# Optimization experiments

Hardware: AMD Instinct MI355X
Metric: run time of the kernel (lower is better)

The kernel has to match this reference:

```python
import jax, jax.numpy as jnp
import numpy as np

B, L, D, H = 2, 1024, 1024, 16
DH = D // H
E, ES, K = 32, 128, 4
LN_EPS = 1e-5


def sinusoidal_pos(length, d):
    # relative offsets length-1 .. -(length-1), Transformer-XL convention
    pos = jnp.arange(length - 1, -length, -1, dtype=jnp.float32)  # [2L-1]
    inv = jnp.exp(-jnp.arange(0, d, 2, dtype=jnp.float32) * (np.log(10000.0) / d))
    ang = pos[:, None] * inv[None, :]
    return jnp.concatenate([jnp.sin(ang), jnp.cos(ang)], axis=-1)  # [2L-1, D]


def layer_norm(x, g, b):
    m = jnp.mean(x, -1, keepdims=True)
    v = jnp.mean(jnp.square(x - m), -1, keepdims=True)
    return (x - m) * jax.lax.rsqrt(v + LN_EPS) * g + b


def rel_attention(x, Wq, Wk, Wv, Wo, Wp):
    q = (x @ Wq).reshape(B, L, H, DH).transpose(0, 2, 1, 3)
    k = (x @ Wk).reshape(B, L, H, DH).transpose(0, 2, 1, 3)
    v = (x @ Wv).reshape(B, L, H, DH).transpose(0, 2, 1, 3)
    p = (sinusoidal_pos(L, D) @ Wp).reshape(2 * L - 1, H, DH).transpose(1, 0, 2)  # [H,2L-1,DH]
    ac = jnp.einsum('bhid,bhjd->bhij', q, k)            # content score
    bd = jnp.einsum('bhid,hpd->bhip', q, p)             # position score [B,H,L,2L-1]
    # offset index of key j relative to query i: pos array index = j - i + (L-1)
    idx = jnp.arange(L)[None, :] - jnp.arange(L)[:, None] + (L - 1)  # [L,L]
    bd = jnp.take_along_axis(bd, jnp.broadcast_to(idx[None, None], (B, H, L, L)), axis=-1)
    att = jax.nn.softmax((ac + bd) / np.sqrt(DH), axis=-1)
    out = jnp.einsum('bhij,bhjd->bhid', att, v).transpose(0, 2, 1, 3).reshape(B, L, D)
    return out @ Wo


def moe_ffn(x, sel_w, keys, values):
    t = x.reshape(-1, D)                                # [T, D]
    gates = jax.nn.sigmoid(t @ sel_w)                   # [T, E]
    topv, topi = jax.lax.top_k(gates, K)                # top-k expert selection
    gate = jnp.zeros_like(gates).at[jnp.arange(t.shape[0])[:, None], topi].set(topv)
    h = jax.nn.relu(jnp.einsum('td,edh->teh', t, keys))  # expert up-proj + ReLU
    y = jnp.einsum('teh,te,ehd->td', h, gate, values)    # gated expert down-proj
    return y.reshape(x.shape)


def setup_inputs():
    key = jax.random.key(0)
    ks = jax.random.split(key, 9)
    s = 0.02
    f32 = jnp.float32
    return {
        'src': jax.random.normal(ks[0], (B, L, D), f32),
        'Wq': jax.random.normal(ks[1], (D, D), f32) * s,
        'Wk': jax.random.normal(ks[2], (D, D), f32) * s,
        'Wv': jax.random.normal(ks[3], (D, D), f32) * s,
        'Wo': jax.random.normal(ks[4], (D, D), f32) * s,
        'Wp': jax.random.normal(ks[5], (D, D), f32) * s,
        'ln1_g': jnp.ones((D,), f32),
        'ln1_b': jnp.zeros((D,), f32),
        'ln2_g': jnp.ones((D,), f32),
        'ln2_b': jnp.zeros((D,), f32),
        'sel_w': jax.random.normal(ks[6], (D, E), f32) * s,
        'keys': jax.random.normal(ks[7], (E, D, ES), f32) * s,
        'values': jax.random.normal(ks[8], (E, ES, D), f32) * s,
    }


def reference(src, Wq, Wk, Wv, Wo, Wp, ln1_g, ln1_b, ln2_g, ln2_b, sel_w, keys, values):
    # pre-LN: attn block
    x2 = layer_norm(src, ln1_g, ln1_b)
    x = src + rel_attention(x2, Wq, Wk, Wv, Wo, Wp)
    # pre-LN: MoE FFN block
    x2 = layer_norm(x, ln2_g, ln2_b)
    return x + moe_ffn(x2, sel_w, keys, values)
```

## Files before the change

### kernel.cpp

```cpp
#include <hip/hip_runtime.h>
#include <hip/hip_bf16.h>
#include <cmath>

typedef __attribute__((ext_vector_type(8))) short s16x8;
typedef __attribute__((ext_vector_type(8))) __bf16 bf16x8;
typedef __attribute__((ext_vector_type(4))) float f32x4;

__device__ __forceinline__ float b2f(short u) {
  union { unsigned int u32; float f; } c;
  c.u32 = ((unsigned int)(unsigned short)u) << 16;
  return c.f;
}
__device__ __forceinline__ short f2b(float f) {
  __hip_bfloat16 h = __float2bfloat16(f);
  return *reinterpret_cast<short*>(&h);
}

__device__ __forceinline__ f32x4 mfma16(bf16x8 a, bf16x8 b, f32x4 c) {
  return __builtin_amdgcn_mfma_f32_16x16x32_bf16(a, b, c, 0, 0, 0);
}

__global__ __launch_bounds__(256) void conv_k(const float* __restrict__ in,
                                              short* __restrict__ out, int n) {
  int stride = gridDim.x << 8;
  for (int i = (blockIdx.x << 8) + threadIdx.x; i < n; i += stride)
    out[i] = f2b(in[i]);
}

__global__ __launch_bounds__(256) void pos_k(short* __restrict__ out) {
  int row = blockIdx.x;
  int t = threadIdx.x;
#pragma unroll
  for (int i = 0; i < 4; ++i) {
    int c = t + (i << 8);
    float val = 0.f;
    if (row < 2047) {
      int f = (c < 512) ? c : c - 512;
      float inv = expf(-(float)f * (float)(9.210340371976184 / 512.0));
      float ang = (float)(1023 - row) * inv;
      val = (c < 512) ? sinf(ang) : cosf(ang);
    }
    out[row * 1024 + c] = f2b(val);
  }
}

__global__ __launch_bounds__(256) void ln_k(const float* __restrict__ in,
                                            const float* __restrict__ g,
                                            const float* __restrict__ bb,
                                            short* __restrict__ out) {
  int row = blockIdx.x;
  int t = threadIdx.x;
  float v[4];
#pragma unroll
  for (int i = 0; i < 4; ++i) v[i] = in[row * 1024 + t + (i << 8)];
  __shared__ float red1[4], red2[4];
  float s = v[0] + v[1] + v[2] + v[3];
#pragma unroll
  for (int m = 1; m < 64; m <<= 1) s += __shfl_xor(s, m);
  if ((t & 63) == 0) red1[t >> 6] = s;
  __syncthreads();
  float mean = (red1[0] + red1[1] + red1[2] + red1[3]) * (1.f / 1024.f);
  float d2 = 0.f;
#pragma unroll
  for (int i = 0; i < 4; ++i) { float d = v[i] - mean; d2 += d * d; }
#pragma unroll
  for (int m = 1; m < 64; m <<= 1) d2 += __shfl_xor(d2, m);
  if ((t & 63) == 0) red2[t >> 6] = d2;
  __syncthreads();
  float var = (red2[0] + red2[1] + red2[2] + red2[3]) * (1.f / 1024.f);
  float rstd = rsqrtf(var + 1e-5f);
#pragma unroll
  for (int i = 0; i < 4; ++i) {
    int c = t + (i << 8);
    out[row * 1024 + c] = f2b((v[i] - mean) * rstd * g[c] + bb[c]);
  }
}

#define GD 1024
template <int EP>
__global__ __launch_bounds__(256) void gemm_k(const short* __restrict__ A,
                                              const short* __restrict__ B,
                                              void* __restrict__ outp,
                                              const float* __restrict__ resid) {
  __shared__ __align__(16) short lA[64 * 40];
  __shared__ __align__(16) short lB[64 * 40];
  const int tid = threadIdx.x;
  const int wave = tid >> 6, lane = tid & 63;
  const int wr = wave >> 1, wc = wave & 1;
  const int m0 = blockIdx.y * 64, n0 = blockIdx.x * 64;
  f32x4 acc[2][2] = {};
  const int ar = tid >> 2, ak = (tid & 3) << 3;
  const int bk = tid >> 3, bn = (tid & 7) << 3;
  const int k8 = (lane >> 4) << 3;
  const int rA0 = wr * 32 + (lane & 15);
  const int cB0 = wc * 32 + (lane & 15);
  for (int kt = 0; kt < GD; kt += 32) {
    *(bf16x8*)&lA[ar * 40 + ak] = *(const bf16x8*)&A[(m0 + ar) * GD + kt + ak];
    s16x8 bv = *(const s16x8*)&B[(kt + bk) * GD + n0 + bn];
#pragma unroll
    for (int i = 0; i < 8; ++i) lB[(bn + i) * 40 + bk] = bv[i];
    __syncthreads();
    bf16x8 a0 = *(bf16x8*)&lA[rA0 * 40 + k8];
    bf16x8 a1 = *(bf16x8*)&lA[(rA0 + 16) * 40 + k8];
    bf16x8 b0 = *(bf16x8*)&lB[cB0 * 40 + k8];
    bf16x8 b1 = *(bf16x8*)&lB[(cB0 + 16) * 40 + k8];
    acc[0][0] = mfma16(a0, b0, acc[0][0]);
    acc[0][1] = mfma16(a0, b1, acc[0][1]);
    acc[1][0] = mfma16(a1, b0, acc[1][0]);
    acc[1][1] = mfma16(a1, b1, acc[1][1]);
    __syncthreads();
  }
#pragma unroll
  for (int mi = 0; mi < 2; ++mi)
#pragma unroll
    for (int ni = 0; ni < 2; ++ni)
#pragma unroll
      for (int r = 0; r < 4; ++r) {
        int row = m0 + wr * 32 + mi * 16 + ((lane >> 4) << 2) + r;
        int col = n0 + wc * 32 + ni * 16 + (lane & 15);
        float vv = acc[mi][ni][r];
        if (EP == 0) {
          ((short*)outp)[row * GD + col] = f2b(vv);
        } else if (EP == 1) {
          int b = row >> 10, l = row & 1023, h = col >> 6, dh = col & 63;
          ((short*)outp)[(((b << 4) + h) * 1024 + l) * 64 + dh] = f2b(vv);
        } else {
          ((float*)outp)[row * GD + col] = vv + resid[row * GD + col];
        }
      }
}

#define KP 72
#define VP 72
#define PBP 72
#define TP 84
#define SPP 72
__global__ __launch_bounds__(256) void attn_k(const short* __restrict__ q,
                                              const short* __restrict__ k,
                                              const short* __restrict__ v,
                                              const short* __restrict__ P,
                                              short* __restrict__ out) {
  __shared__ __align__(16) short sK[64 * KP];
  __shared__ __align__(16) short sVT[64 * VP];
  __shared__ __align__(16) short sPB[128 * PBP];
  __shared__ __align__(16) float sT[4 * 16 * TP];
  __shared__ __align__(16) short sP[4 * 16 * SPP];

  const int bx = blockIdx.x;
  const int bh = bx >> 4;
  const int chunk = bx & 15;
  const int b = bh >> 4, h = bh & 15;
  const int i0 = chunk << 6;
  const int t = threadIdx.x;
  const int w = t >> 6;
  const int lane = t & 63;
  const int cl = lane & 15;
  const int g = lane >> 4;
  const size_t base = (size_t)bh << 16;
  const short* qb = q + base;
  const short* kb = k + base;
  const short* vb = v + base;

  bf16x8 qf[2];
  {
    const short* qr = qb + (i0 + w * 16 + cl) * 64 + g * 8;
    qf[0] = *(const bf16x8*)&qr[0];
    qf[1] = *(const bf16x8*)&qr[32];
  }

  f32x4 acc_o[4] = {};
  float m_reg[4], l_reg[4];
#pragma unroll
  for (int r = 0; r < 4; ++r) { m_reg[r] = -1e30f; l_reg[r] = 0.f; }

  float* sTw = sT + w * (16 * TP);
  short* sPw = sP + w * (16 * SPP);
  const int a_row = g * 4;
  const int prow0 = 48 - w * 16 + cl;

  for (int j0 = 0; j0 < 1024; j0 += 64) {
    __syncthreads();
    {
      int c0 = t << 1;
#pragma unroll
      for (int u = 0; u < 2; ++u) {
        int c = c0 + u;
        int row = c >> 3, col8 = (c & 7) << 3;
        *(s16x8*)&sK[row * KP + col8] = *(const s16x8*)&kb[(j0 + row) * 64 + col8];
        s16x8 vv = *(const s16x8*)&vb[(j0 + row) * 64 + col8];
#pragma unroll
        for (int e = 0; e < 8; ++e) sVT[(col8 + e) * VP + row] = vv[e];
      }
      int ob = 960 - i0 + j0;
#pragma unroll
      for (int u = 0; u < 4; ++u) {
        int c = t + (u << 8);
        int row = c >> 3, col8 = (c & 7) << 3;
        *(s16x8*)&sPB[row * PBP + col8] =
            *(const s16x8*)&P[(size_t)(ob + row) * 1024 + (h << 6) + col8];
      }
    }
    __syncthreads();

    f32x4 acc_s[4] = {};
    f32x4 acc_t[5] = {};
#pragma unroll
    for (int kk = 0; kk < 2; ++kk) {
      bf16x8 a = qf[kk];
      int koff = kk * 32 + g * 8;
#pragma unroll
      for (int nj = 0; nj < 4; ++nj) {
        bf16x8 bfr = *(const bf16x8*)&sK[(nj * 16 + cl) * KP + koff];
        acc_s[nj] = mfma16(a, bfr, acc_s[nj]);
      }
#pragma unroll
      for (int nt = 0; nt < 5; ++nt) {
        bf16x8 bfr = *(const bf16x8*)&sPB[(prow0 + nt * 16) * PBP + koff];
        acc_t[nt] = mfma16(a, bfr, acc_t[nt]);
      }
    }
#pragma unroll
    for (int nt = 0; nt < 5; ++nt)
#pragma unroll
      for (int r = 0; r < 4; ++r)
        sTw[(a_row + r) * TP + nt * 16 + cl] = acc_t[nt][r];

    float sval[4][4];
#pragma unroll
    for (int r = 0; r < 4; ++r) {
      int a = a_row + r;
      int abase = a * (TP - 1) + 15 + cl;
      float mr = -1e30f;
#pragma unroll
      for (int ni = 0; ni < 4; ++ni) {
        float sv = (acc_s[ni][r] + sTw[abase + ni * 16]) * 0.125f;
        sval[r][ni] = sv;
        mr = fmaxf(mr, sv);
      }
      mr = fmaxf(mr, __shfl_xor(mr, 1));
      mr = fmaxf(mr, __shfl_xor(mr, 2));
      mr = fmaxf(mr, __shfl_xor(mr, 4));
      mr = fmaxf(mr, __shfl_xor(mr, 8));
      float nm = fmaxf(m_reg[r], mr);
      float sc = __expf(m_reg[r] - nm);
      m_reg[r] = nm;
      float ls = 0.f;
#pragma unroll
      for (int ni = 0; ni < 4; ++ni) {
        float p = __expf(sval[r][ni] - nm);
        sval[r][ni] = p;
        ls += p;
      }
      ls += __shfl_xor(ls, 1);
      ls += __shfl_xor(ls, 2);
      ls += __shfl_xor(ls, 4);
      ls += __shfl_xor(ls, 8);
      l_reg[r] = l_reg[r] * sc + ls;
#pragma unroll
      for (int nd = 0; nd < 4; ++nd) acc_o[nd][r] *= sc;
#pragma unroll
      for (int ni = 0; ni < 4; ++ni)
        sPw[a * SPP + ni * 16 + cl] = f2b(sval[r][ni]);
    }

#pragma unroll
    for (int kk = 0; kk < 2; ++kk) {
      int koff = kk * 32 + g * 8;
      bf16x8 a = *(const bf16x8*)&sPw[cl * SPP + koff];
#pragma unroll
      for (int nd = 0; nd < 4; ++nd) {
        bf16x8 bfr = *(const bf16x8*)&sVT[(nd * 16 + cl) * VP + koff];
        acc_o[nd] = mfma16(a, bfr, acc_o[nd]);
      }
    }
  }
  {
    int orow = b * 1024 + i0 + w * 16 + a_row;
#pragma unroll
    for (int r = 0; r < 4; ++r) {
      float rl = 1.f / l_reg[r];
      int row = orow + r;
#pragma unroll
      for (int nd = 0; nd < 4; ++nd)
        out[row * 1024 + (h << 6) + nd * 16 + cl] = f2b(acc_o[nd][r] * rl);
    }
  }
}

__global__ __launch_bounds__(256) void gate_k(const float* __restrict__ x,
                                              const float* __restrict__ g,
                                              const float* __restrict__ bb,
                                              const float* __restrict__ selw,
                                              float* __restrict__ topv,
                                              int* __restrict__ topi) {
  int tok = blockIdx.x;
  int t = threadIdx.x;
  __shared__ float sT[1024];
  __shared__ float red1[4], red2[4];
  __shared__ float sG[32];
  float v[4];
#pragma unroll
  for (int i = 0; i < 4; ++i) v[i] = x[tok * 1024 + t + (i << 8)];
  float s = v[0] + v[1] + v[2] + v[3];
#pragma unroll
  for (int m = 1; m < 64; m <<= 1) s += __shfl_xor(s, m);
  if ((t & 63) == 0) red1[t >> 6] = s;
  __syncthreads();
  float mean = (red1[0] + red1[1] + red1[2] + red1[3]) * (1.f / 1024.f);
  float d2 = 0.f;
#pragma unroll
  for (int i = 0; i < 4; ++i) { float d = v[i] - mean; d2 += d * d; }
#pragma unroll
  for (int m = 1; m < 64; m <<= 1) d2 += __shfl_xor(d2, m);
  if ((t & 63) == 0) red2[t >> 6] = d2;
  __syncthreads();
  float var = (red2[0] + red2[1] + red2[2] + red2[3]) * (1.f / 1024.f);
  float rstd = rsqrtf(var + 1e-5f);
#pragma unroll
  for (int i = 0; i < 4; ++i) {
    int c = t + (i << 8);
    sT[c] = (v[i] - mean) * rstd * g[c] + bb[c];
  }
  __syncthreads();
  if (t < 32) {
    float acc = 0.f;
    for (int d = 0; d < 1024; ++d) acc += sT[d] * selw[d * 32 + t];
    sG[t] = acc;
  }
  __syncthreads();
  if (t == 0) {
    bool used[32];
    for (int e = 0; e < 32; ++e) used[e] = false;
    for (int kk = 0; kk < 4; ++kk) {
      int bi = 0;
      float bvv = -1e30f;
      for (int e = 0; e < 32; ++e)
        if (!used[e] && sG[e] > bvv) { bvv = sG[e]; bi = e; }
      used[bi] = true;
      topi[tok * 4 + kk] = bi;
      topv[tok * 4 + kk] = 1.f / (1.f + __expf(-bvv));
    }
  }
}

#define CAP 2048
__global__ __launch_bounds__(32) void zero_k(int* __restrict__ cnt) {
  cnt[threadIdx.x] = 0;
}
__global__ __launch_bounds__(256) void bucket_k(const int* __restrict__ topi,
                                                const float* __restrict__ topv,
                                                int* __restrict__ cnt,
                                                int* __restrict__ toklist,
                                                float* __restrict__ gatelist) {
  int tok = (blockIdx.x << 8) + threadIdx.x;
#pragma unroll
  for (int kk = 0; kk < 4; ++kk) {
    int e = topi[tok * 4 + kk];
    float gv = topv[tok * 4 + kk];
    int pos = atomicAdd(&cnt[e], 1);
    toklist[e * CAP + pos] = tok;
    gatelist[e * CAP + pos] = gv;
  }
}

__global__ __launch_bounds__(256) void cp_k(const float* __restrict__ in,
                                            float* __restrict__ out) {
  int i = (blockIdx.x << 8) + threadIdx.x;
  *(f32x4*)&out[i << 2] = *(const f32x4*)&in[i << 2];
}

__global__ __launch_bounds__(256) void moe_up_k(const short* __restrict__ x2,
                                                const short* __restrict__ keys,
                                                const int* __restrict__ cnt,
                                                const int* __restrict__ toklist,
                                                short* __restrict__ hbuf) {
  const int e = blockIdx.y;
  const int n = cnt[e];
  const int t0 = blockIdx.x << 6;
  if (t0 >= n) return;
  __shared__ int stok[64];
  __shared__ __align__(16) short lA[64 * 36];
  __shared__ __align__(16) short lB[128 * 36];
  const int tid = threadIdx.x;
  if (tid < 64) {
    int idx = t0 + tid;
    stok[tid] = toklist[e * CAP + (idx < n ? idx : n - 1)];
  }
  __syncthreads();
  const int w = tid >> 6, lane = tid & 63, cl = lane & 15, g = lane >> 4;
  const int ar = tid >> 2, ak = (tid & 3) << 3;
  const int bkr = tid >> 3, bc0 = (tid & 7) << 4;
  const short* kbase = keys + ((size_t)e << 17);
  f32x4 acc[8] = {};
  for (int kt = 0; kt < 1024; kt += 32) {
    if (kt) __syncthreads();
    *(s16x8*)&lA[ar * 36 + ak] = *(const s16x8*)&x2[stok[ar] * 1024 + kt + ak];
    {
      s16x8 b0 = *(const s16x8*)&kbase[(kt + bkr) * 128 + bc0];
      s16x8 b1 = *(const s16x8*)&kbase[(kt + bkr) * 128 + bc0 + 8];
#pragma unroll
      for (int i2 = 0; i2 < 8; ++i2) {
        lB[(bc0 + i2) * 36 + bkr] = b0[i2];
        lB[(bc0 + 8 + i2) * 36 + bkr] = b1[i2];
      }
    }
    __syncthreads();
    bf16x8 a = *(const bf16x8*)&lA[(w * 16 + cl) * 36 + g * 8];
#pragma unroll
    for (int nt = 0; nt < 8; ++nt) {
      bf16x8 bfr = *(const bf16x8*)&lB[(nt * 16 + cl) * 36 + g * 8];
      acc[nt] = mfma16(a, bfr, acc[nt]);
    }
  }
#pragma unroll
  for (int nt = 0; nt < 8; ++nt)
#pragma unroll
    for (int r = 0; r < 4; ++r) {
      int lrow = w * 16 + g * 4 + r;
      if (t0 + lrow < n)
        hbuf[(size_t)(e * CAP + t0 + lrow) * 128 + nt * 16 + cl] =
            f2b(fmaxf(acc[nt][r], 0.f));
    }
}

__global__ __launch_bounds__(256) void moe_down_k(const short* __restrict__ hbuf,
                                                  const short* __restrict__ vals,
                                                  const int* __restrict__ cnt,
                                                  const int* __restrict__ toklist,
                                                  const float* __restrict__ gatelist,
                                                  float* __restrict__ out) {
  const int e = blockIdx.y;
  const int n = cnt[e];
  const int t0 = blockIdx.x << 6;
  if (t0 >= n) return;
  __shared__ int stok[64];
  __shared__ float sgate[64];
  __shared__ __align__(16) short lA[64 * 132];
  __shared__ __align__(16) short lB[64 * 132];
  const int tid = threadIdx.x;
  if (tid < 64) {
    int idx = t0 + tid;
    int ci = idx < n ? idx : n - 1;
    stok[tid] = toklist[e * CAP + ci];
    sgate[tid] = gatelist[e * CAP + ci];
  }
  {
    int ar = tid >> 2, ac0 = (tid & 3) << 3;
    const short* hr = &hbuf[(size_t)(e * CAP + t0 + ar) * 128];
#pragma unroll
    for (int u = 0; u < 4; ++u)
      *(s16x8*)&lA[ar * 132 + ac0 + u * 32] = *(const s16x8*)&hr[ac0 + u * 32];
  }
  const int w = tid >> 6, lane = tid & 63, cl = lane & 15, g = lane >> 4;
  const short* vbase = vals + ((size_t)e << 17);
  const int bkr = tid >> 1, bc0 = (tid & 1) << 5;
  __syncthreads();
  bf16x8 afr[4];
#pragma unroll
  for (int ks = 0; ks < 4; ++ks)
    afr[ks] = *(const bf16x8*)&lA[(w * 16 + cl) * 132 + ks * 32 + g * 8];
  float gates[4];
  int stokr[4];
  bool valid[4];
#pragma unroll
  for (int r = 0; r < 4; ++r) {
    int lrow = w * 16 + g * 4 + r;
    gates[r] = sgate[lrow];
    stokr[r] = stok[lrow];
    valid[r] = (t0 + lrow) < n;
  }
  for (int nc = 0; nc < 16; ++nc) {
    __syncthreads();
#pragma unroll
    for (int u = 0; u < 4; ++u) {
      s16x8 bv = *(const s16x8*)&vbase[bkr * 1024 + nc * 64 + bc0 + u * 8];
#pragma unroll
      for (int i2 = 0; i2 < 8; ++i2) lB[(bc0 + u * 8 + i2) * 132 + bkr] = bv[i2];
    }
    __syncthreads();
    f32x4 acc[4] = {};
#pragma unroll
    for (int ks = 0; ks < 4; ++ks)
#pragma unroll
      for (int nt = 0; nt < 4; ++nt) {
        bf16x8 bfr = *(const bf16x8*)&lB[(nt * 16 + cl) * 132 + ks * 32 + g * 8];
        acc[nt] = mfma16(afr[ks], bfr, acc[nt]);
      }
#pragma unroll
    for (int nt = 0; nt < 4; ++nt)
#pragma unroll
      for (int r = 0; r < 4; ++r)
        if (valid[r])
          atomicAdd(&out[stokr[r] * 1024 + nc * 64 + nt * 16 + cl],
                    gates[r] * acc[nt][r]);
  }
}

extern "C" void kernel_launch(void* const* d_in, const int* in_sizes, int n_in,
                              void* d_out, int out_size, void* d_ws, size_t ws_size,
                              hipStream_t stream) {
  const float* src = (const float*)d_in[0];
  const float* ln1g = (const float*)d_in[6];
  const float* ln1b = (const float*)d_in[7];
  const float* ln2g = (const float*)d_in[8];
  const float* ln2b = (const float*)d_in[9];
  const float* selw = (const float*)d_in[10];

  char* ws = (char*)d_ws;
  short* x2a = (short*)(ws + (size_t)0);
  short* pos = (short*)(ws + ((size_t)4 << 20));
  short* P = (short*)(ws + ((size_t)8 << 20));
  short* q = (short*)(ws + ((size_t)12 << 20));
  short* k = (short*)(ws + ((size_t)16 << 20));
  short* v = (short*)(ws + ((size_t)20 << 20));
  short* ao = (short*)(ws + ((size_t)24 << 20));
  short* x2b = (short*)(ws + ((size_t)28 << 20));
  float* x = (float*)(ws + ((size_t)32 << 20));
  float* topv = (float*)(ws + ((size_t)40 << 20));
  int* topi = (int*)(ws + ((size_t)40 << 20) + (32 << 10));
  short* cWq = (short*)(ws + ((size_t)41 << 20));
  short* cWk = (short*)(ws + ((size_t)43 << 20));
  short* cWv = (short*)(ws + ((size_t)45 << 20));
  short* cWo = (short*)(ws + ((size_t)47 << 20));
  short* cWp = (short*)(ws + ((size_t)49 << 20));
  short* cKeys = (short*)(ws + ((size_t)51 << 20));
  short* cVals = (short*)(ws + ((size_t)59 << 20));
  short* hbuf = q;
  int* cnt = (int*)(ws + ((size_t)4 << 20));
  int* toklist = (int*)(ws + ((size_t)4 << 20) + (4 << 10));
  float* gatelist = (float*)(ws + ((size_t)4 << 20) + (512 << 10));

  conv_k<<<512, 256, 0, stream>>>((const float*)d_in[1], cWq, 1048576);
  conv_k<<<512, 256, 0, stream>>>((const float*)d_in[2], cWk, 1048576);
  conv_k<<<512, 256, 0, stream>>>((const float*)d_in[3], cWv, 1048576);
  conv_k<<<512, 256, 0, stream>>>((const float*)d_in[4], cWo, 1048576);
  conv_k<<<512, 256, 0, stream>>>((const float*)d_in[5], cWp, 1048576);
  conv_k<<<1024, 256, 0, stream>>>((const float*)d_in[11], cKeys, 4194304);
  conv_k<<<1024, 256, 0, stream>>>((const float*)d_in[12], cVals, 4194304);

  dim3 gg(16, 32);
  pos_k<<<2048, 256, 0, stream>>>(pos);
  ln_k<<<2048, 256, 0, stream>>>(src, ln1g, ln1b, x2a);
  gemm_k<1><<<gg, 256, 0, stream>>>(x2a, cWq, q, nullptr);
  gemm_k<1><<<gg, 256, 0, stream>>>(x2a, cWk, k, nullptr);
  gemm_k<1><<<gg, 256, 0, stream>>>(x2a, cWv, v, nullptr);
  gemm_k<0><<<gg, 256, 0, stream>>>(pos, cWp, P, nullptr);
  attn_k<<<512, 256, 0, stream>>>(q, k, v, P, ao);
  gemm_k<2><<<gg, 256, 0, stream>>>(ao, cWo, x, src);
  ln_k<<<2048, 256, 0, stream>>>(x, ln2g, ln2b, x2b);
  gate_k<<<2048, 256, 0, stream>>>(x, ln2g, ln2b, selw, topv, topi);
  zero_k<<<1, 32, 0, stream>>>(cnt);
  bucket_k<<<8, 256, 0, stream>>>(topi, topv, cnt, toklist, gatelist);
  cp_k<<<2048, 256, 0, stream>>>(x, (float*)d_out);
  moe_up_k<<<dim3(32, 32), 256, 0, stream>>>(x2b, cKeys, cnt, toklist, hbuf);
  moe_down_k<<<dim3(32, 32), 256, 0, stream>>>(hbuf, cVals, cnt, toklist, gatelist,
                                               (float*)d_out);
}
```

Baseline: 566.7 us.

## Pre-transpose MoE expert weights and load MFMA fragments directly from global memory

Expert keys and values are now converted to bf16 in a transposed layout through a new shared-memory tiled transpose kernel. This lets the MoE up and down kernels read MFMA operand fragments straight from global memory with contiguous 16-byte loads, removing the LDS staging, the scalar transposing stores and the barriers. The down-projection also splits output columns across a new grid dimension (8 chunks of 128), giving more parallel blocks. In exchange there is no LDS reuse of the B operand across waves, so more global and L2 traffic, and the transpose kernel adds some preprocessing cost.

```diff
diff --git a/kernel.cpp b/kernel.cpp
--- a/kernel.cpp
+++ b/kernel.cpp
@@ -25,6 +25,23 @@
   int stride = gridDim.x << 8;
   for (int i = (blockIdx.x << 8) + threadIdx.x; i < n; i += stride)
     out[i] = f2b(in[i]);
+}
+
+__global__ __launch_bounds__(256) void convT_k(const float* __restrict__ in,
+                                               short* __restrict__ out, int R, int C) {
+  __shared__ float s[32][33];
+  int e = blockIdx.z;
+  int r0 = blockIdx.y << 5, c0 = blockIdx.x << 5;
+  int tx = threadIdx.x & 31, ty = threadIdx.x >> 5;
+  const float* ib = in + (size_t)e * R * C;
+  short* ob = out + (size_t)e * C * R;
+#pragma unroll
+  for (int u = 0; u < 4; ++u)
+    s[ty + u * 8][tx] = ib[(size_t)(r0 + ty + u * 8) * C + c0 + tx];
+  __syncthreads();
+#pragma unroll
+  for (int u = 0; u < 4; ++u)
+    ob[(size_t)(c0 + ty + u * 8) * R + r0 + tx] = f2b(s[tx][ty + u * 8]);
 }
 
 __global__ __launch_bounds__(256) void pos_k(short* __restrict__ out) {
@@ -370,7 +387,7 @@
 }
 
 __global__ __launch_bounds__(256) void moe_up_k(const short* __restrict__ x2,
-                                                const short* __restrict__ keys,
+                                                const short* __restrict__ kT,
                                                 const int* __restrict__ cnt,
                                                 const int* __restrict__ toklist,
                                                 short* __restrict__ hbuf) {
@@ -378,121 +395,72 @@
   const int n = cnt[e];
   const int t0 = blockIdx.x << 6;
   if (t0 >= n) return;
-  __shared__ int stok[64];
-  __shared__ __align__(16) short lA[64 * 36];
-  __shared__ __align__(16) short lB[128 * 36];
   const int tid = threadIdx.x;
-  if (tid < 64) {
-    int idx = t0 + tid;
-    stok[tid] = toklist[e * CAP + (idx < n ? idx : n - 1)];
-  }
-  __syncthreads();
   const int w = tid >> 6, lane = tid & 63, cl = lane & 15, g = lane >> 4;
-  const int ar = tid >> 2, ak = (tid & 3) << 3;
-  const int bkr = tid >> 3, bc0 = (tid & 7) << 4;
-  const short* kbase = keys + ((size_t)e << 17);
+  int arow = t0 + w * 16 + cl;
+  int atok = toklist[e * CAP + (arow < n ? arow : n - 1)];
+  const short* aptr = x2 + (size_t)atok * 1024 + g * 8;
+  const short* bptr = kT + ((size_t)e << 17) + cl * 1024 + g * 8;
   f32x4 acc[8] = {};
+#pragma unroll 4
   for (int kt = 0; kt < 1024; kt += 32) {
-    if (kt) __syncthreads();
-    *(s16x8*)&lA[ar * 36 + ak] = *(const s16x8*)&x2[stok[ar] * 1024 + kt + ak];
-    {
-      s16x8 b0 = *(const s16x8*)&kbase[(kt + bkr) * 128 + bc0];
-      s16x8 b1 = *(const s16x8*)&kbase[(kt + bkr) * 128 + bc0 + 8];
-#pragma unroll
-      for (int i2 = 0; i2 < 8; ++i2) {
-        lB[(bc0 + i2) * 36 + bkr] = b0[i2];
-        lB[(bc0 + 8 + i2) * 36 + bkr] = b1[i2];
-      }
-    }
-    __syncthreads();
-    bf16x8 a = *(const bf16x8*)&lA[(w * 16 + cl) * 36 + g * 8];
+    bf16x8 a = *(const bf16x8*)&aptr[kt];
 #pragma unroll
     for (int nt = 0; nt < 8; ++nt) {
-      bf16x8 bfr = *(const bf16x8*)&lB[(nt * 16 + cl) * 36 + g * 8];
-      acc[nt] = mfma16(a, bfr, acc[nt]);
-    }
-  }
-#pragma unroll
-  for (int nt = 0; nt < 8; ++nt)
-#pragma unroll
-    for (int r = 0; r < 4; ++r) {
-      int lrow = w * 16 + g * 4 + r;
-      if (t0 + lrow < n)
-        hbuf[(size_t)(e * CAP + t0 + lrow) * 128 + nt * 16 + cl] =
-            f2b(fmaxf(acc[nt][r], 0.f));
-    }
+      bf16x8 b = *(const bf16x8*)&bptr[nt * 16384 + kt];
+      acc[nt] = mfma16(a, b, acc[nt]);
+    }
+  }
+  int sr0 = t0 + w * 16 + g * 4;
+#pragma unroll
+  for (int r = 0; r < 4; ++r) {
+    int sr = sr0 + r;
+    if (sr < n) {
+      short* hp = &hbuf[((size_t)e * CAP + sr) * 128 + cl];
+#pragma unroll
+      for (int nt = 0; nt < 8; ++nt) hp[nt * 16] = f2b(fmaxf(acc[nt][r], 0.f));
+    }
+  }
 }
 
 __global__ __launch_bounds__(256) void moe_down_k(const short* __restrict__ hbuf,
-                                                  const short* __restrict__ vals,
+                                                  const short* __restrict__ vT,
                                                   const int* __restrict__ cnt,
                                                   const int* __restrict__ toklist,
                                                   const float* __restrict__ gatelist,
                                                   float* __restrict__ out) {
-  const int e = blockIdx.y;
+  const int e = blockIdx.z;
   const int n = cnt[e];
-  const int t0 = blockIdx.x << 6;
+  const int t0 = blockIdx.y << 6;
   if (t0 >= n) return;
-  __shared__ int stok[64];
-  __shared__ float sgate[64];
-  __shared__ __align__(16) short lA[64 * 132];
-  __shared__ __align__(16) short lB[64 * 132];
+  const int nc0 = blockIdx.x << 7;
   const int tid = threadIdx.x;
-  if (tid < 64) {
-    int idx = t0 + tid;
-    int ci = idx < n ? idx : n - 1;
-    stok[tid] = toklist[e * CAP + ci];
-    sgate[tid] = gatelist[e * CAP + ci];
-  }
-  {
-    int ar = tid >> 2, ac0 = (tid & 3) << 3;
-    const short* hr = &hbuf[(size_t)(e * CAP + t0 + ar) * 128];
-#pragma unroll
-    for (int u = 0; u < 4; ++u)
-      *(s16x8*)&lA[ar * 132 + ac0 + u * 32] = *(const s16x8*)&hr[ac0 + u * 32];
-  }
   const int w = tid >> 6, lane = tid & 63, cl = lane & 15, g = lane >> 4;
-  const short* vbase = vals + ((size_t)e << 17);
-  const int bkr = tid >> 1, bc0 = (tid & 1) << 5;
-  __syncthreads();
-  bf16x8 afr[4];
-#pragma unroll
-  for (int ks = 0; ks < 4; ++ks)
-    afr[ks] = *(const bf16x8*)&lA[(w * 16 + cl) * 132 + ks * 32 + g * 8];
-  float gates[4];
-  int stokr[4];
-  bool valid[4];
+  int arow = t0 + w * 16 + cl;
+  int arc = arow < n ? arow : n - 1;
+  const short* aptr = hbuf + ((size_t)e * CAP + arc) * 128 + g * 8;
+  const short* bptr = vT + ((size_t)e << 17) + (size_t)(nc0 + cl) * 128 + g * 8;
+  f32x4 acc[8] = {};
+#pragma unroll
+  for (int ks = 0; ks < 4; ++ks) {
+    bf16x8 a = *(const bf16x8*)&aptr[ks * 32];
+#pragma unroll
+    for (int nt = 0; nt < 8; ++nt) {
+      bf16x8 b = *(const bf16x8*)&bptr[nt * 2048 + ks * 32];
+      acc[nt] = mfma16(a, b, acc[nt]);
+    }
+  }
+  int sr0 = t0 + w * 16 + g * 4;
 #pragma unroll
   for (int r = 0; r < 4; ++r) {
-    int lrow = w * 16 + g * 4 + r;
-    gates[r] = sgate[lrow];
-    stokr[r] = stok[lrow];
-    valid[r] = (t0 + lrow) < n;
-  }
-  for (int nc = 0; nc < 16; ++nc) {
-    __syncthreads();
-#pragma unroll
-    for (int u = 0; u < 4; ++u) {
-      s16x8 bv = *(const s16x8*)&vbase[bkr * 1024 + nc * 64 + bc0 + u * 8];
-#pragma unroll
-      for (int i2 = 0; i2 < 8; ++i2) lB[(bc0 + u * 8 + i2) * 132 + bkr] = bv[i2];
-    }
-    __syncthreads();
-    f32x4 acc[4] = {};
-#pragma unroll
-    for (int ks = 0; ks < 4; ++ks)
-#pragma unroll
-      for (int nt = 0; nt < 4; ++nt) {
-        bf16x8 bfr = *(const bf16x8*)&lB[(nt * 16 + cl) * 132 + ks * 32 + g * 8];
-        acc[nt] = mfma16(afr[ks], bfr, acc[nt]);
-      }
-#pragma unroll
-    for (int nt = 0; nt < 4; ++nt)
-#pragma unroll
-      for (int r = 0; r < 4; ++r)
-        if (valid[r])
-          atomicAdd(&out[stokr[r] * 1024 + nc * 64 + nt * 16 + cl],
-                    gates[r] * acc[nt][r]);
+    int sr = sr0 + r;
+    if (sr < n) {
+      int tok = toklist[e * CAP + sr];
+      float gv = gatelist[e * CAP + sr];
+      float* op = &out[(size_t)tok * 1024 + nc0 + cl];
+#pragma unroll
+      for (int nt = 0; nt < 8; ++nt) atomicAdd(&op[nt * 16], gv * acc[nt][r]);
+    }
   }
 }
 
@@ -523,8 +491,8 @@
   short* cWv = (short*)(ws + ((size_t)45 << 20));
   short* cWo = (short*)(ws + ((size_t)47 << 20));
   short* cWp = (short*)(ws + ((size_t)49 << 20));
-  short* cKeys = (short*)(ws + ((size_t)51 << 20));
-  short* cVals = (short*)(ws + ((size_t)59 << 20));
+  short* cKeysT = (short*)(ws + ((size_t)51 << 20));
+  short* cValsT = (short*)(ws + ((size_t)59 << 20));
   short* hbuf = q;
   int* cnt = (int*)(ws + ((size_t)4 << 20));
   int* toklist = (int*)(ws + ((size_t)4 << 20) + (4 << 10));
@@ -535,8 +503,8 @@
   conv_k<<<512, 256, 0, stream>>>((const float*)d_in[3], cWv, 1048576);
   conv_k<<<512, 256, 0, stream>>>((const float*)d_in[4], cWo, 1048576);
   conv_k<<<512, 256, 0, stream>>>((const float*)d_in[5], cWp, 1048576);
-  conv_k<<<1024, 256, 0, stream>>>((const float*)d_in[11], cKeys, 4194304);
-  conv_k<<<1024, 256, 0, stream>>>((const float*)d_in[12], cVals, 4194304);
+  convT_k<<<dim3(4, 32, 32), 256, 0, stream>>>((const float*)d_in[11], cKeysT, 1024, 128);
+  convT_k<<<dim3(32, 4, 32), 256, 0, stream>>>((const float*)d_in[12], cValsT, 128, 1024);
 
   dim3 gg(16, 32);
   pos_k<<<2048, 256, 0, stream>>>(pos);
@@ -552,7 +520,7 @@
   zero_k<<<1, 32, 0, stream>>>(cnt);
   bucket_k<<<8, 256, 0, stream>>>(topi, topv, cnt, toklist, gatelist);
   cp_k<<<2048, 256, 0, stream>>>(x, (float*)d_out);
-  moe_up_k<<<dim3(32, 32), 256, 0, stream>>>(x2b, cKeys, cnt, toklist, hbuf);
-  moe_down_k<<<dim3(32, 32), 256, 0, stream>>>(hbuf, cVals, cnt, toklist, gatelist,
-                                               (float*)d_out);
-}
+  moe_up_k<<<dim3(32, 32), 256, 0, stream>>>(x2b, cKeysT, cnt, toklist, hbuf);
+  moe_down_k<<<dim3(8, 32, 32), 256, 0, stream>>>(hbuf, cValsT, cnt, toklist, gatelist,
+                                                  (float*)d_out);
+}
```

New measurement: 597.7 us. 1.05x slower.
